# Performance work log

Hardware: AMD Instinct MI355X
Metric: run time of the kernel (lower is better)

Reference implementation:

```python
import jax, jax.numpy as jnp
import numpy as np

B, C, L = 2048, 9605, 8
ALPHA = 0.5        # self.alpha
ALPHA1 = 0.05      # margin
ALPHA2 = 2.0       # asymmetric scale when violated
ALPHA3 = 5.0       # logistic sharpness
ALPHA_OTHER = 0.3  # floor on top-k threshold
TOPK = 16          # x_sorted[15] -> 16th largest


def setup_inputs() -> dict:
    key = jax.random.key(0)
    k1, k2, k3, k4 = jax.random.split(key, 4)
    x = jax.random.normal(k1, (B, C), dtype=jnp.float32)
    # each class assigned to one of 5*L slots; slots < L are whitelist groups,
    # the rest are 'other' classes (like total_indices in the torch code)
    gid = jax.random.randint(k4, (C,), 0, 5 * L)
    gid = gid.at[:L].set(jnp.arange(L))  # guarantee every group is non-empty
    group_mask = gid[None, :] == jnp.arange(L)[:, None]  # [L, C] bool
    # sparse multi-label binarized targets (~14 positives/sample)
    y = (jax.random.uniform(k2, (B, C)) < 0.0015).astype(jnp.float32)
    y_neg = (jax.random.uniform(k3, (B, C)) < 0.0015).astype(jnp.float32)
    return {"x": x, "y": y, "y_neg": y_neg, "group_mask": group_mask}


def _rank_loss(x1, x2):
    # our_rank_loss: sigmoid(alpha3*(x2-x1+margin)), scaled by alpha2 when violated
    d = x2 - x1 + ALPHA1
    s = jax.nn.sigmoid(ALPHA3 * d)
    return jnp.where(d > 0, ALPHA2 * s, s)


def reference(x, y, y_neg, group_mask):
    xs = jax.nn.sigmoid(x)  # [B, C]
    # top_k_thres = max(16th-largest sigmoid score, alpha_other)
    thres = jnp.maximum(jax.lax.top_k(xs, TOPK)[0][:, TOPK - 1], ALPHA_OTHER)  # [B]
    maskf = group_mask.astype(xs.dtype)  # [L, C]
    neg_inf = jnp.array(-jnp.inf, xs.dtype)
    # per-sample max score inside each whitelist group: [B, L]
    group_max = jnp.max(jnp.where(group_mask[None, :, :], xs[:, None, :], neg_inf), axis=-1)
    # find_gt_whitelist: group is 'hit' if any positive target inside it
    gt = (y @ maskf.T) > 0        # [B, L]
    gt_neg = (y_neg @ maskf.T) > 0  # [B, L]
    has_gt = jnp.any(gt, axis=-1)    # [B]; False <=> sentinel len(all_labels)
    has_neg = jnp.any(gt_neg, axis=-1)
    # ---- case B: sample hits at least one whitelist group ----
    rl_correct = _rank_loss(group_max, thres[:, None])    # gt groups above thres
    rl_incorrect = _rank_loss(thres[:, None], group_max)  # non-gt groups below thres
    caseB = jnp.sum(jnp.where(gt, rl_correct, rl_incorrect), axis=-1)  # [B]
    # ---- case A: no whitelist group hit ----
    union = jnp.any(group_mask, axis=0)  # [C] union of all whitelist classes
    union_max = jnp.max(jnp.where(union[None, :], xs, neg_inf), axis=-1)  # [B]
    neg_max = jnp.max(jnp.where(gt_neg, group_max, neg_inf), axis=-1)
    neg_score = jnp.where(has_neg, neg_max, jnp.zeros((), xs.dtype))  # torch starts at 0
    caseA = (1.0 - ALPHA) * _rank_loss(thres, union_max) + ALPHA * _rank_loss(thres, neg_score)
    loss_rank_all = jnp.where(has_gt, caseB, caseA)  # [B]
    return jnp.mean(loss_rank_all)
```

## Files before the change

kernel.cpp:

```cpp
#include <hip/hip_runtime.h>
#include <math.h>

constexpr int B_ = 2048;
constexpr int C_ = 9605;
constexpr int L_ = 8;
constexpr int TOPK_ = 16;
constexpr int CAP_ = 1024;
constexpr float T0_ = 2.0f;

__device__ __forceinline__ float sigm(float v) { return 1.0f / (1.0f + expf(-v)); }

__device__ __forceinline__ float rank_loss(float x1, float x2) {
  float d = x2 - x1 + 0.05f;
  float s = 1.0f / (1.0f + expf(-5.0f * d));
  return (d > 0.0f) ? 2.0f * s : s;
}

__device__ __forceinline__ unsigned int fkey(float v) {
  unsigned int u = __float_as_uint(v);
  return u ^ ((u & 0x80000000u) ? 0xFFFFFFFFu : 0x80000000u);
}
__device__ __forceinline__ float fkeyinv(unsigned int k) {
  unsigned int u = (k & 0x80000000u) ? (k ^ 0x80000000u) : ~k;
  return __uint_as_float(u);
}

__global__ void build_code_kernel(const int* __restrict__ mask,
                                  unsigned char* __restrict__ code) {
  int c = blockIdx.x * 256 + threadIdx.x;
  if (c >= C_) return;
  unsigned char cd = 0xFF;
#pragma unroll
  for (int l = L_ - 1; l >= 0; --l)
    if (mask[l * C_ + c] != 0) cd = (unsigned char)l;
  code[c] = cd;
}

__global__ void __launch_bounds__(256) row_loss_kernel(
    const float* __restrict__ x, const float* __restrict__ y,
    const float* __restrict__ yn, const unsigned char* __restrict__ code,
    float* __restrict__ loss) {
  __shared__ float slot[L_ * 256];
  __shared__ float cand[CAP_];
  __shared__ int cand_cnt;
  __shared__ unsigned int gt_bits, gtn_bits;
  __shared__ float s_x16;
  __shared__ int s_red;

  const int t = threadIdx.x;
  const int b = blockIdx.x;
  const float* xr = x + (size_t)b * C_;
  const float* yr = y + (size_t)b * C_;
  const float* ynr = yn + (size_t)b * C_;

#pragma unroll
  for (int l = 0; l < L_; ++l) slot[(l << 8) + t] = -INFINITY;
  if (t == 0) { cand_cnt = 0; gt_bits = 0u; gtn_bits = 0u; }
  __syncthreads();

  auto elem = [&](int , unsigned char cd, float xv, float yv, float ynv) {
    if (cd < L_) {
      int a = ((int)cd << 8) + t;
      if (xv > slot[a]) slot[a] = xv;
      if (yv > 0.0f) atomicOr(&gt_bits, 1u << cd);
      if (ynv > 0.0f) atomicOr(&gtn_bits, 1u << cd);
    }
    if (xv > T0_) {
      int p = atomicAdd(&cand_cnt, 1);
      if (p < CAP_) cand[p] = xv;
    }
  };

  const int lead = (4 - ((b * C_) & 3)) & 3;
  const int n4 = (C_ - lead) >> 2;
  for (int j = t; j < n4; j += 256) {
    int c0 = lead + (j << 2);
    float4 xv = *reinterpret_cast<const float4*>(xr + c0);
    float4 yv = *reinterpret_cast<const float4*>(yr + c0);
    float4 nv = *reinterpret_cast<const float4*>(ynr + c0);
    unsigned char d0 = code[c0], d1 = code[c0 + 1], d2 = code[c0 + 2], d3 = code[c0 + 3];
    elem(c0,     d0, xv.x, yv.x, nv.x);
    elem(c0 + 1, d1, xv.y, yv.y, nv.y);
    elem(c0 + 2, d2, xv.z, yv.z, nv.z);
    elem(c0 + 3, d3, xv.w, yv.w, nv.w);
  }
  for (int c = t; c < lead; c += 256) elem(c, code[c], xr[c], yr[c], ynr[c]);
  for (int c = lead + (n4 << 2) + t; c < C_; c += 256) elem(c, code[c], xr[c], yr[c], ynr[c]);
  __syncthreads();

  for (int s = 128; s > 0; s >>= 1) {
    if (t < s) {
#pragma unroll
      for (int l = 0; l < L_; ++l) {
        float o = slot[(l << 8) + t + s];
        if (o > slot[(l << 8) + t]) slot[(l << 8) + t] = o;
      }
    }
    __syncthreads();
  }

  const int cnt = cand_cnt;
  const bool mainp = (cnt >= TOPK_) && (cnt <= CAP_);
  if (mainp) {
    if (t < 64) {
      unsigned int ku[CAP_ / 64];
#pragma unroll
      for (int k = 0; k < CAP_ / 64; ++k) {
        int idx = t + (k << 6);
        ku[k] = (idx < cnt) ? fkey(cand[idx]) : 0u;
      }
      unsigned int lo = 0u, hi = 0xFFFFFFFFu;
      for (int it = 0; it < 32 && lo < hi; ++it) {
        unsigned int mid = lo + ((hi - lo) >> 1) + 1u;
        int c16 = 0;
#pragma unroll
        for (int k = 0; k < CAP_ / 64; ++k) c16 += (ku[k] >= mid) ? 1 : 0;
#pragma unroll
        for (int off = 32; off > 0; off >>= 1) c16 += __shfl_xor(c16, off, 64);
        if (c16 >= TOPK_) lo = mid; else hi = mid - 1u;
      }
      if (t == 0) s_x16 = fkeyinv(lo);
    }
  } else {
    unsigned int lo = 0u, hi = 0xFFFFFFFFu;
    for (int it = 0; it < 32; ++it) {
      if (lo >= hi) break;
      unsigned int mid = lo + ((hi - lo) >> 1) + 1u;
      if (t == 0) s_red = 0;
      __syncthreads();
      int cl = 0;
      for (int c = t; c < C_; c += 256) cl += (fkey(xr[c]) >= mid) ? 1 : 0;
      atomicAdd(&s_red, cl);
      __syncthreads();
      int total = s_red;
      __syncthreads();
      if (total >= TOPK_) lo = mid; else hi = mid - 1u;
    }
    if (t == 0) s_x16 = fkeyinv(lo);
  }
  __syncthreads();

  if (t == 0) {
    float thres = fmaxf(sigm(s_x16), 0.3f);
    unsigned int gtb = gt_bits, gnb = gtn_bits;
    float caseB = 0.0f, unio = -INFINITY, negmax = -INFINITY;
#pragma unroll
    for (int l = 0; l < L_; ++l) {
      float g = sigm(slot[l << 8]);
      unio = fmaxf(unio, g);
      caseB += ((gtb >> l) & 1u) ? rank_loss(g, thres) : rank_loss(thres, g);
      if ((gnb >> l) & 1u) negmax = fmaxf(negmax, g);
    }
    float negscore = (gnb != 0u) ? negmax : 0.0f;
    float caseA = 0.5f * rank_loss(thres, unio) + 0.5f * rank_loss(thres, negscore);
    loss[b] = (gtb != 0u) ? caseB : caseA;
  }
}

__global__ void mean_kernel(const float* __restrict__ loss, float* __restrict__ out) {
  const int t = threadIdx.x;
  float s = 0.0f;
  for (int i = t; i < B_; i += 256) s += loss[i];
#pragma unroll
  for (int off = 32; off > 0; off >>= 1) s += __shfl_xor(s, off, 64);
  __shared__ float part[4];
  if ((t & 63) == 0) part[t >> 6] = s;
  __syncthreads();
  if (t == 0) out[0] = (part[0] + part[1] + part[2] + part[3]) * (1.0f / (float)B_);
}

extern "C" void kernel_launch(void* const* d_in, const int* in_sizes, int n_in,
                              void* d_out, int out_size, void* d_ws, size_t ws_size,
                              hipStream_t stream) {
  const float* x = (const float*)d_in[0];
  const float* y = (const float*)d_in[1];
  const float* yn = (const float*)d_in[2];
  const int* mask = (const int*)d_in[3];

  float* loss = (float*)d_ws;
  unsigned char* code = (unsigned char*)d_ws + B_ * sizeof(float);

  hipLaunchKernelGGL(build_code_kernel, dim3((C_ + 255) / 256), dim3(256), 0, stream,
                     mask, code);
  hipLaunchKernelGGL(row_loss_kernel, dim3(B_), dim3(256), 0, stream,
                     x, y, yn, code, loss);
  hipLaunchKernelGGL(mean_kernel, dim3(1), dim3(256), 0, stream,
                     loss, (float*)d_out);
}
```

Baseline: 255.9 us.

## Keep group maxima and candidates in registers, reduce via wave shuffles

Per-thread group maxima, label bitmasks and up to 8 top-k candidates now live in registers rather than shared memory with per-element atomics. They are combined with wave shuffles and a per-wave shared-memory slot, which removes the 8-step shared-memory tree reduction and the contended atomics in the hot loop. A new pre-pass packs class codes into 4 phase-shifted uint32 arrays so each thread loads one aligned word per float4 instead of four byte loads. Candidate capacity is halved, and any thread overflowing its 8 slots forces the slow full-row binary-search fallback.

```diff
diff --git a/kernel.cpp b/kernel.cpp
--- a/kernel.cpp
+++ b/kernel.cpp
@@ -5,8 +5,10 @@
 constexpr int C_ = 9605;
 constexpr int L_ = 8;
 constexpr int TOPK_ = 16;
-constexpr int CAP_ = 1024;
+constexpr int CAP_ = 512;
+constexpr int NSLOT_ = 8;
 constexpr float T0_ = 2.0f;
+constexpr int QW_ = 2404;
 
 __device__ __forceinline__ float sigm(float v) { return 1.0f / (1.0f + expf(-v)); }
 
@@ -36,14 +38,30 @@
   code[c] = cd;
 }
 
+__global__ void pack_code_kernel(const unsigned char* __restrict__ code,
+                                 unsigned int* __restrict__ codeq) {
+  int k = blockIdx.x * 256 + threadIdx.x;
+  int r = blockIdx.y;
+  if (k >= QW_) return;
+  unsigned int v = 0u;
+#pragma unroll
+  for (int e = 0; e < 4; ++e) {
+    int c = r + 4 * k + e;
+    unsigned int byte = (c < C_) ? (unsigned int)code[c] : 0xFFu;
+    v |= byte << (8 * e);
+  }
+  codeq[r * QW_ + k] = v;
+}
+
 __global__ void __launch_bounds__(256) row_loss_kernel(
     const float* __restrict__ x, const float* __restrict__ y,
     const float* __restrict__ yn, const unsigned char* __restrict__ code,
-    float* __restrict__ loss) {
-  __shared__ float slot[L_ * 256];
+    const unsigned int* __restrict__ codeq, float* __restrict__ loss) {
   __shared__ float cand[CAP_];
   __shared__ int cand_cnt;
-  __shared__ unsigned int gt_bits, gtn_bits;
+  __shared__ int s_of;
+  __shared__ float wgm[4][L_];
+  __shared__ unsigned int wgt[4], wgn[4];
   __shared__ float s_x16;
   __shared__ int s_red;
 
@@ -53,54 +71,86 @@
   const float* yr = y + (size_t)b * C_;
   const float* ynr = yn + (size_t)b * C_;
 
-#pragma unroll
-  for (int l = 0; l < L_; ++l) slot[(l << 8) + t] = -INFINITY;
-  if (t == 0) { cand_cnt = 0; gt_bits = 0u; gtn_bits = 0u; }
-  __syncthreads();
-
-  auto elem = [&](int , unsigned char cd, float xv, float yv, float ynv) {
-    if (cd < L_) {
-      int a = ((int)cd << 8) + t;
-      if (xv > slot[a]) slot[a] = xv;
-      if (yv > 0.0f) atomicOr(&gt_bits, 1u << cd);
-      if (ynv > 0.0f) atomicOr(&gtn_bits, 1u << cd);
-    }
-    if (xv > T0_) {
-      int p = atomicAdd(&cand_cnt, 1);
-      if (p < CAP_) cand[p] = xv;
-    }
+  if (t == 0) { cand_cnt = 0; s_of = 0; }
+
+  float gm[L_];
+#pragma unroll
+  for (int l = 0; l < L_; ++l) gm[l] = -INFINITY;
+  unsigned int gtb = 0u, gnb = 0u;
+  float cnd[NSLOT_];
+  int cc = 0;
+#pragma unroll
+  for (int k = 0; k < NSLOT_; ++k) cnd[k] = -INFINITY;
+
+  auto proc = [&](float xv, float yv, float nv, int cd) {
+#pragma unroll
+    for (int l = 0; l < L_; ++l)
+      if (cd == l) gm[l] = fmaxf(gm[l], xv);
+    unsigned int mb = (cd < L_) ? (1u << (cd & 7)) : 0u;
+    gtb |= (yv > 0.0f) ? mb : 0u;
+    gnb |= (nv > 0.0f) ? mb : 0u;
+    int cci = (xv > T0_) ? cc : NSLOT_;
+#pragma unroll
+    for (int k = 0; k < NSLOT_; ++k)
+      if (cci == k) cnd[k] = xv;
+    cc += (xv > T0_) ? 1 : 0;
   };
 
-  const int lead = (4 - ((b * C_) & 3)) & 3;
+  const int r = b & 3;
+  const int lead = (4 - r) & 3;
   const int n4 = (C_ - lead) >> 2;
-  for (int j = t; j < n4; j += 256) {
-    int c0 = lead + (j << 2);
-    float4 xv = *reinterpret_cast<const float4*>(xr + c0);
-    float4 yv = *reinterpret_cast<const float4*>(yr + c0);
-    float4 nv = *reinterpret_cast<const float4*>(ynr + c0);
-    unsigned char d0 = code[c0], d1 = code[c0 + 1], d2 = code[c0 + 2], d3 = code[c0 + 3];
-    elem(c0,     d0, xv.x, yv.x, nv.x);
-    elem(c0 + 1, d1, xv.y, yv.y, nv.y);
-    elem(c0 + 2, d2, xv.z, yv.z, nv.z);
-    elem(c0 + 3, d3, xv.w, yv.w, nv.w);
-  }
-  for (int c = t; c < lead; c += 256) elem(c, code[c], xr[c], yr[c], ynr[c]);
-  for (int c = lead + (n4 << 2) + t; c < C_; c += 256) elem(c, code[c], xr[c], yr[c], ynr[c]);
-  __syncthreads();
-
-  for (int s = 128; s > 0; s >>= 1) {
-    if (t < s) {
-#pragma unroll
-      for (int l = 0; l < L_; ++l) {
-        float o = slot[(l << 8) + t + s];
-        if (o > slot[(l << 8) + t]) slot[(l << 8) + t] = o;
-      }
-    }
-    __syncthreads();
-  }
+  const float4* x4 = reinterpret_cast<const float4*>(x) + (((size_t)b * C_ + lead) >> 2);
+  const float4* y4 = reinterpret_cast<const float4*>(y) + (((size_t)b * C_ + lead) >> 2);
+  const float4* v4 = reinterpret_cast<const float4*>(yn) + (((size_t)b * C_ + lead) >> 2);
+  const unsigned int* cq = codeq + lead * QW_;
+
+  for (int k = t; k < n4; k += 256) {
+    float4 xv = x4[k];
+    float4 yv = y4[k];
+    float4 nv = v4[k];
+    unsigned int cqk = cq[k];
+    proc(xv.x, yv.x, nv.x, (int)(cqk & 0xFF));
+    proc(xv.y, yv.y, nv.y, (int)((cqk >> 8) & 0xFF));
+    proc(xv.z, yv.z, nv.z, (int)((cqk >> 16) & 0xFF));
+    proc(xv.w, yv.w, nv.w, (int)((cqk >> 24) & 0xFF));
+  }
+  if (t < lead) proc(xr[t], yr[t], ynr[t], (int)code[t]);
+  const int tstart = lead + (n4 << 2);
+  if (t >= 4 && t < 4 + (C_ - tstart)) {
+    int c = tstart + (t - 4);
+    proc(xr[c], yr[c], ynr[c], (int)code[c]);
+  }
+
+#pragma unroll
+  for (int off = 32; off > 0; off >>= 1) {
+#pragma unroll
+    for (int l = 0; l < L_; ++l) gm[l] = fmaxf(gm[l], __shfl_xor(gm[l], off, 64));
+    gtb |= (unsigned int)__shfl_xor((int)gtb, off, 64);
+    gnb |= (unsigned int)__shfl_xor((int)gnb, off, 64);
+  }
+
+  __syncthreads();
+
+  int nw = (cc < NSLOT_) ? cc : NSLOT_;
+  if (nw > 0) {
+    int pos = atomicAdd(&cand_cnt, nw);
+#pragma unroll
+    for (int k = 0; k < NSLOT_; ++k)
+      if (k < nw && pos + k < CAP_) cand[pos + k] = cnd[k];
+  }
+  if (cc > NSLOT_) atomicOr(&s_of, 1);
+
+  if ((t & 63) == 0) {
+    int w = t >> 6;
+#pragma unroll
+    for (int l = 0; l < L_; ++l) wgm[w][l] = gm[l];
+    wgt[w] = gtb;
+    wgn[w] = gnb;
+  }
+  __syncthreads();
 
   const int cnt = cand_cnt;
-  const bool mainp = (cnt >= TOPK_) && (cnt <= CAP_);
+  const bool mainp = (cnt >= TOPK_) && (cnt <= CAP_) && (s_of == 0);
   if (mainp) {
     if (t < 64) {
       unsigned int ku[CAP_ / 64];
@@ -142,18 +192,20 @@
 
   if (t == 0) {
     float thres = fmaxf(sigm(s_x16), 0.3f);
-    unsigned int gtb = gt_bits, gnb = gtn_bits;
+    unsigned int gtbf = wgt[0] | wgt[1] | wgt[2] | wgt[3];
+    unsigned int gnbf = wgn[0] | wgn[1] | wgn[2] | wgn[3];
     float caseB = 0.0f, unio = -INFINITY, negmax = -INFINITY;
 #pragma unroll
     for (int l = 0; l < L_; ++l) {
-      float g = sigm(slot[l << 8]);
+      float gx = fmaxf(fmaxf(wgm[0][l], wgm[1][l]), fmaxf(wgm[2][l], wgm[3][l]));
+      float g = sigm(gx);
       unio = fmaxf(unio, g);
-      caseB += ((gtb >> l) & 1u) ? rank_loss(g, thres) : rank_loss(thres, g);
-      if ((gnb >> l) & 1u) negmax = fmaxf(negmax, g);
+      caseB += ((gtbf >> l) & 1u) ? rank_loss(g, thres) : rank_loss(thres, g);
+      if ((gnbf >> l) & 1u) negmax = fmaxf(negmax, g);
     }
-    float negscore = (gnb != 0u) ? negmax : 0.0f;
+    float negscore = (gnbf != 0u) ? negmax : 0.0f;
     float caseA = 0.5f * rank_loss(thres, unio) + 0.5f * rank_loss(thres, negscore);
-    loss[b] = (gtb != 0u) ? caseB : caseA;
+    loss[b] = (gtbf != 0u) ? caseB : caseA;
   }
 }
 
@@ -178,12 +230,15 @@
   const int* mask = (const int*)d_in[3];
 
   float* loss = (float*)d_ws;
-  unsigned char* code = (unsigned char*)d_ws + B_ * sizeof(float);
+  unsigned char* code = (unsigned char*)d_ws + 8192;
+  unsigned int* codeq = (unsigned int*)((char*)d_ws + 8192 + 9612);
 
   hipLaunchKernelGGL(build_code_kernel, dim3((C_ + 255) / 256), dim3(256), 0, stream,
                      mask, code);
+  hipLaunchKernelGGL(pack_code_kernel, dim3((QW_ + 255) / 256, 4), dim3(256), 0, stream,
+                     code, codeq);
   hipLaunchKernelGGL(row_loss_kernel, dim3(B_), dim3(256), 0, stream,
-                     x, y, yn, code, loss);
+                     x, y, yn, code, codeq, loss);
   hipLaunchKernelGGL(mean_kernel, dim3(1), dim3(256), 0, stream,
                      loss, (float*)d_out);
 }
```

After: 262.0 us. 2.4% more time.

## Gather group maxima via precomputed index lists and use wave-level reductions

Applied to the files above, without the earlier changes.

Adds a kernel that builds a fixed-size per-group list of class indices. The row kernel then computes each group's max by gathering two entries per thread from that list, instead of per-thread shared-memory slot updates followed by a tree reduction. Target-bit accumulation moves from shared atomics to per-thread registers combined with wave shuffles. The main loop is unrolled with nontemporal float4 loads and skips groups of four with a max pre-check. This assumes every group has at most 512 members (GSEG), and the candidate buffer is halved to 512.

```diff
diff --git a/kernel.cpp b/kernel.cpp
--- a/kernel.cpp
+++ b/kernel.cpp
@@ -5,8 +5,11 @@
 constexpr int C_ = 9605;
 constexpr int L_ = 8;
 constexpr int TOPK_ = 16;
-constexpr int CAP_ = 1024;
+constexpr int CAP_ = 512;
 constexpr float T0_ = 2.0f;
+constexpr int GSEG_ = 512;
+
+typedef float vfloat4 __attribute__((ext_vector_type(4)));
 
 __device__ __forceinline__ float sigm(float v) { return 1.0f / (1.0f + expf(-v)); }
 
@@ -36,68 +39,139 @@
   code[c] = cd;
 }
 
+__global__ void build_glist_kernel(const unsigned char* __restrict__ code,
+                                   unsigned int* __restrict__ glist) {
+  __shared__ int cnt;
+  __shared__ unsigned int firstidx;
+  const int l = blockIdx.x;
+  const int t = threadIdx.x;
+  if (t == 0) { cnt = 0; firstidx = 0u; }
+  __syncthreads();
+  for (int c = t; c < C_; c += 256) {
+    if (code[c] == (unsigned char)l) {
+      int p = atomicAdd(&cnt, 1);
+      if (p < GSEG_) glist[l * GSEG_ + p] = (unsigned int)c;
+      if (p == 0) firstidx = (unsigned int)c;
+    }
+  }
+  __syncthreads();
+  int n = (cnt < GSEG_) ? cnt : GSEG_;
+  unsigned int f = firstidx;
+  for (int s = n + t; s < GSEG_; s += 256) glist[l * GSEG_ + s] = f;
+}
+
 __global__ void __launch_bounds__(256) row_loss_kernel(
     const float* __restrict__ x, const float* __restrict__ y,
     const float* __restrict__ yn, const unsigned char* __restrict__ code,
-    float* __restrict__ loss) {
-  __shared__ float slot[L_ * 256];
+    const unsigned int* __restrict__ glist, float* __restrict__ loss) {
   __shared__ float cand[CAP_];
   __shared__ int cand_cnt;
-  __shared__ unsigned int gt_bits, gtn_bits;
+  __shared__ float wgm[4][L_];
+  __shared__ unsigned int wgt[4], wgn[4];
   __shared__ float s_x16;
   __shared__ int s_red;
 
   const int t = threadIdx.x;
   const int b = blockIdx.x;
-  const float* xr = x + (size_t)b * C_;
-  const float* yr = y + (size_t)b * C_;
-  const float* ynr = yn + (size_t)b * C_;
-
-#pragma unroll
-  for (int l = 0; l < L_; ++l) slot[(l << 8) + t] = -INFINITY;
-  if (t == 0) { cand_cnt = 0; gt_bits = 0u; gtn_bits = 0u; }
-  __syncthreads();
-
-  auto elem = [&](int , unsigned char cd, float xv, float yv, float ynv) {
-    if (cd < L_) {
-      int a = ((int)cd << 8) + t;
-      if (xv > slot[a]) slot[a] = xv;
-      if (yv > 0.0f) atomicOr(&gt_bits, 1u << cd);
-      if (ynv > 0.0f) atomicOr(&gtn_bits, 1u << cd);
-    }
-    if (xv > T0_) {
-      int p = atomicAdd(&cand_cnt, 1);
-      if (p < CAP_) cand[p] = xv;
-    }
-  };
-
-  const int lead = (4 - ((b * C_) & 3)) & 3;
+  const size_t rb = (size_t)b * C_;
+  const float* xr = x + rb;
+  const float* yr = y + rb;
+  const float* nr = yn + rb;
+  if (t == 0) cand_cnt = 0;
+  __syncthreads();
+
+  unsigned int gtb = 0u, gnb = 0u;
+
+  auto cappend = [&](float v) {
+    int p = atomicAdd(&cand_cnt, 1);
+    if (p < CAP_) cand[p] = v;
+  };
+  auto candq = [&](vfloat4 v) {
+    float m = fmaxf(fmaxf(v.x, v.y), fmaxf(v.z, v.w));
+    if (m > T0_) {
+      if (v.x > T0_) cappend(v.x);
+      if (v.y > T0_) cappend(v.y);
+      if (v.z > T0_) cappend(v.z);
+      if (v.w > T0_) cappend(v.w);
+    }
+  };
+  auto posq = [&](vfloat4 v, int c0, unsigned int& bits) {
+    float m = fmaxf(fmaxf(v.x, v.y), fmaxf(v.z, v.w));
+    if (m > 0.0f) {
+      if (v.x > 0.0f) { unsigned char cd = code[c0];     if (cd < L_) bits |= 1u << cd; }
+      if (v.y > 0.0f) { unsigned char cd = code[c0 + 1]; if (cd < L_) bits |= 1u << cd; }
+      if (v.z > 0.0f) { unsigned char cd = code[c0 + 2]; if (cd < L_) bits |= 1u << cd; }
+      if (v.w > 0.0f) { unsigned char cd = code[c0 + 3]; if (cd < L_) bits |= 1u << cd; }
+    }
+  };
+  auto scalar_elem = [&](int c) {
+    float v = xr[c];
+    if (v > T0_) cappend(v);
+    if (yr[c] > 0.0f) { unsigned char cd = code[c]; if (cd < L_) gtb |= 1u << cd; }
+    if (nr[c] > 0.0f) { unsigned char cd = code[c]; if (cd < L_) gnb |= 1u << cd; }
+  };
+
+  const int lead = (4 - (b & 3)) & 3;
   const int n4 = (C_ - lead) >> 2;
-  for (int j = t; j < n4; j += 256) {
-    int c0 = lead + (j << 2);
-    float4 xv = *reinterpret_cast<const float4*>(xr + c0);
-    float4 yv = *reinterpret_cast<const float4*>(yr + c0);
-    float4 nv = *reinterpret_cast<const float4*>(ynr + c0);
-    unsigned char d0 = code[c0], d1 = code[c0 + 1], d2 = code[c0 + 2], d3 = code[c0 + 3];
-    elem(c0,     d0, xv.x, yv.x, nv.x);
-    elem(c0 + 1, d1, xv.y, yv.y, nv.y);
-    elem(c0 + 2, d2, xv.z, yv.z, nv.z);
-    elem(c0 + 3, d3, xv.w, yv.w, nv.w);
-  }
-  for (int c = t; c < lead; c += 256) elem(c, code[c], xr[c], yr[c], ynr[c]);
-  for (int c = lead + (n4 << 2) + t; c < C_; c += 256) elem(c, code[c], xr[c], yr[c], ynr[c]);
-  __syncthreads();
-
-  for (int s = 128; s > 0; s >>= 1) {
-    if (t < s) {
-#pragma unroll
-      for (int l = 0; l < L_; ++l) {
-        float o = slot[(l << 8) + t + s];
-        if (o > slot[(l << 8) + t]) slot[(l << 8) + t] = o;
-      }
-    }
-    __syncthreads();
-  }
+  const vfloat4* x4 = reinterpret_cast<const vfloat4*>(x) + ((rb + lead) >> 2);
+  const vfloat4* y4 = reinterpret_cast<const vfloat4*>(y) + ((rb + lead) >> 2);
+  const vfloat4* v4 = reinterpret_cast<const vfloat4*>(yn) + ((rb + lead) >> 2);
+
+  for (int kb = 0; kb < 2048; kb += 1024) {
+    int k0 = kb + t, k1 = k0 + 256, k2 = k0 + 512, k3 = k0 + 768;
+    vfloat4 a0 = __builtin_nontemporal_load(x4 + k0);
+    vfloat4 a1 = __builtin_nontemporal_load(x4 + k1);
+    vfloat4 a2 = __builtin_nontemporal_load(x4 + k2);
+    vfloat4 a3 = __builtin_nontemporal_load(x4 + k3);
+    vfloat4 b0 = __builtin_nontemporal_load(y4 + k0);
+    vfloat4 b1 = __builtin_nontemporal_load(y4 + k1);
+    vfloat4 b2 = __builtin_nontemporal_load(y4 + k2);
+    vfloat4 b3 = __builtin_nontemporal_load(y4 + k3);
+    vfloat4 c0 = __builtin_nontemporal_load(v4 + k0);
+    vfloat4 c1 = __builtin_nontemporal_load(v4 + k1);
+    vfloat4 c2 = __builtin_nontemporal_load(v4 + k2);
+    vfloat4 c3 = __builtin_nontemporal_load(v4 + k3);
+    candq(a0); candq(a1); candq(a2); candq(a3);
+    posq(b0, lead + 4 * k0, gtb); posq(b1, lead + 4 * k1, gtb);
+    posq(b2, lead + 4 * k2, gtb); posq(b3, lead + 4 * k3, gtb);
+    posq(c0, lead + 4 * k0, gnb); posq(c1, lead + 4 * k1, gnb);
+    posq(c2, lead + 4 * k2, gnb); posq(c3, lead + 4 * k3, gnb);
+  }
+  for (int k = 2048 + t; k < n4; k += 256) {
+    vfloat4 a = __builtin_nontemporal_load(x4 + k);
+    vfloat4 bq = __builtin_nontemporal_load(y4 + k);
+    vfloat4 cq = __builtin_nontemporal_load(v4 + k);
+    candq(a);
+    posq(bq, lead + 4 * k, gtb);
+    posq(cq, lead + 4 * k, gnb);
+  }
+  if (t < lead) scalar_elem(t);
+  const int ts = lead + (n4 << 2);
+  if (t >= 64 && t < 64 + (C_ - ts)) scalar_elem(ts + (t - 64));
+
+  float gm[L_];
+#pragma unroll
+  for (int l = 0; l < L_; ++l) {
+    unsigned int ia = glist[l * GSEG_ + t];
+    unsigned int ib = glist[l * GSEG_ + 256 + t];
+    gm[l] = fmaxf(xr[ia], xr[ib]);
+  }
+
+#pragma unroll
+  for (int off = 32; off > 0; off >>= 1) {
+#pragma unroll
+    for (int l = 0; l < L_; ++l) gm[l] = fmaxf(gm[l], __shfl_xor(gm[l], off, 64));
+    gtb |= (unsigned int)__shfl_xor((int)gtb, off, 64);
+    gnb |= (unsigned int)__shfl_xor((int)gnb, off, 64);
+  }
+  if ((t & 63) == 0) {
+    int w = t >> 6;
+#pragma unroll
+    for (int l = 0; l < L_; ++l) wgm[w][l] = gm[l];
+    wgt[w] = gtb;
+    wgn[w] = gnb;
+  }
+  __syncthreads();
 
   const int cnt = cand_cnt;
   const bool mainp = (cnt >= TOPK_) && (cnt <= CAP_);
@@ -142,18 +216,20 @@
 
   if (t == 0) {
     float thres = fmaxf(sigm(s_x16), 0.3f);
-    unsigned int gtb = gt_bits, gnb = gtn_bits;
+    unsigned int gtbf = wgt[0] | wgt[1] | wgt[2] | wgt[3];
+    unsigned int gnbf = wgn[0] | wgn[1] | wgn[2] | wgn[3];
     float caseB = 0.0f, unio = -INFINITY, negmax = -INFINITY;
 #pragma unroll
     for (int l = 0; l < L_; ++l) {
-      float g = sigm(slot[l << 8]);
+      float gx = fmaxf(fmaxf(wgm[0][l], wgm[1][l]), fmaxf(wgm[2][l], wgm[3][l]));
+      float g = sigm(gx);
       unio = fmaxf(unio, g);
-      caseB += ((gtb >> l) & 1u) ? rank_loss(g, thres) : rank_loss(thres, g);
-      if ((gnb >> l) & 1u) negmax = fmaxf(negmax, g);
-    }
-    float negscore = (gnb != 0u) ? negmax : 0.0f;
+      caseB += ((gtbf >> l) & 1u) ? rank_loss(g, thres) : rank_loss(thres, g);
+      if ((gnbf >> l) & 1u) negmax = fmaxf(negmax, g);
+    }
+    float negscore = (gnbf != 0u) ? negmax : 0.0f;
     float caseA = 0.5f * rank_loss(thres, unio) + 0.5f * rank_loss(thres, negscore);
-    loss[b] = (gtb != 0u) ? caseB : caseA;
+    loss[b] = (gtbf != 0u) ? caseB : caseA;
   }
 }
 
@@ -177,13 +253,17 @@
   const float* yn = (const float*)d_in[2];
   const int* mask = (const int*)d_in[3];
 
-  float* loss = (float*)d_ws;
-  unsigned char* code = (unsigned char*)d_ws + B_ * sizeof(float);
+  char* ws = (char*)d_ws;
+  float* loss = (float*)ws;
+  unsigned char* code = (unsigned char*)(ws + 8192);
+  unsigned int* glist = (unsigned int*)(ws + 8192 + 9632);
 
   hipLaunchKernelGGL(build_code_kernel, dim3((C_ + 255) / 256), dim3(256), 0, stream,
                      mask, code);
+  hipLaunchKernelGGL(build_glist_kernel, dim3(L_), dim3(256), 0, stream,
+                     code, glist);
   hipLaunchKernelGGL(row_loss_kernel, dim3(B_), dim3(256), 0, stream,
-                     x, y, yn, code, loss);
+                     x, y, yn, code, glist, loss);
   hipLaunchKernelGGL(mean_kernel, dim3(1), dim3(256), 0, stream,
                      loss, (float*)d_out);
 }
```

Result: slower. 262.5 us (+2.6%).
